# Performance work log

Measured on AMD Instinct MI355X. Metric: run time of the kernel, lower is better.

## Reference

```python
import jax, jax.numpy as jnp
import numpy as np

WIN = 7
SIZE = 56
HEADS = 16
DIM = 512
SHIFT = WIN // 2  # 3


def _rel_index():
    # Matches torch.meshgrid (ij) + flatten + pairwise diff indexing of the bias table.
    coords = np.stack(np.meshgrid(np.arange(WIN), np.arange(WIN), indexing='ij')).reshape(2, -1)  # [2,49]
    rel = (coords[:, :, None] - coords[:, None, :]).transpose(1, 2, 0)  # [49,49,2]
    rel[..., 0] += WIN - 1
    rel[..., 1] += WIN - 1
    rel[..., 0] *= 2 * WIN - 1
    return (rel[..., 0] + rel[..., 1]).reshape(-1)  # [49*49]


def _attn_mask():
    # Shifted-window mask: windows mixing different regions get -100 on cross pairs.
    img = np.zeros((SIZE, SIZE))
    sl = (slice(0, -WIN), slice(-WIN, -SHIFT), slice(-SHIFT, None))
    cnt = 0
    for h in sl:
        for w in sl:
            img[h, w] = cnt
            cnt += 1
    m = img.reshape(SIZE // WIN, WIN, SIZE // WIN, WIN).transpose(0, 2, 1, 3).reshape(-1, WIN * WIN)  # [nW,49]
    am = m[:, None, :] - m[:, :, None]  # [nW,49,49]
    return np.where(am != 0, -100.0, 0.0).astype(np.float32)


_REL_IDX = _rel_index()
_MASK = _attn_mask()  # [64,49,49]


def setup_inputs() -> dict:
    key = jax.random.key(0)
    ks = jax.random.split(key, 6)
    Bn, N, C = 2048, WIN * WIN, DIM
    return {
        'x': jax.random.normal(ks[0], (Bn, N, C), jnp.float32),
        'qkv_w': jax.random.normal(ks[1], (C, 3 * C), jnp.float32) * (C ** -0.5),
        'qkv_b': jax.random.normal(ks[2], (3 * C,), jnp.float32) * 0.02,
        'proj_w': jax.random.normal(ks[3], (C, C), jnp.float32) * (C ** -0.5),
        'proj_b': jax.random.normal(ks[4], (C,), jnp.float32) * 0.02,
        'bias_table': jax.random.normal(ks[5], ((2 * WIN - 1) ** 2, HEADS), jnp.float32) * 0.02,
    }


def reference(x, qkv_w, qkv_b, proj_w, proj_b, bias_table):
    Bn, N, C = x.shape
    D = C // HEADS
    qkv = (x @ qkv_w + qkv_b).reshape(Bn, N, 3, HEADS, D).transpose(2, 0, 3, 1, 4)  # [3,Bn,H,N,D]
    q, k, v = qkv[0] * (D ** -0.5), qkv[1], qkv[2]
    attn = jnp.einsum('bhnd,bhmd->bhnm', q, k)  # [Bn,H,N,N]
    bias = bias_table[jnp.asarray(_REL_IDX)].reshape(N, N, HEADS).transpose(2, 0, 1)  # [H,N,N]
    attn = attn + bias[None]
    mask = jnp.asarray(_MASK, x.dtype)  # [nW,N,N]
    nW = mask.shape[0]
    attn = attn.reshape(Bn // nW, nW, HEADS, N, N) + mask[None, :, None]
    attn = jax.nn.softmax(attn.reshape(Bn, HEADS, N, N), axis=-1)
    out = jnp.einsum('bhnm,bhmd->bhnd', attn, v).transpose(0, 2, 1, 3).reshape(Bn, N, C)
    return out @ proj_w + proj_b
```

## Files before the change

### kernel.cpp

```cpp
#include <hip/hip_runtime.h>
#include <hip/hip_bf16.h>
#include <stdint.h>


#define HEADS 16
#define NTOK  49
#define CH    512

typedef float  f32x4  __attribute__((ext_vector_type(4)));
typedef __bf16 bf16x8 __attribute__((ext_vector_type(8)));
typedef unsigned short u16;
typedef unsigned int   u32;

__device__ __forceinline__ u16 f2bf(float f) {
  return __builtin_bit_cast(u16, (__bf16)f);
}

__device__ __forceinline__ void gload16(const u16* g, u16* l) {
  __builtin_amdgcn_global_load_lds(
      (const __attribute__((address_space(1))) u32*)g,
      (__attribute__((address_space(3))) u32*)l, 16, 0, 0);
}

__global__ __launch_bounds__(256) void k_wprep(const float* __restrict__ qkv_w,
                                               const float* __restrict__ proj_w,
                                               const float* __restrict__ qkv_b,
                                               u16* __restrict__ Wt, u16* __restrict__ Pt,
                                               float* __restrict__ bias2) {
  const float sc = 0.17677669529663687f;
  int tid = blockIdx.x * 256 + threadIdx.x;
  const int T1 = 1536 * 512;
  if (tid < 1536) bias2[tid] = qkv_b[tid] * (tid < 512 ? sc : 1.f);
  if (tid < T1) {
    int n = tid >> 9, k = tid & 511;
    float v = qkv_w[k * 1536 + n];
    if (n < 512) v *= sc;
    Wt[tid] = f2bf(v);
  } else {
    int t2 = tid - T1;
    int n = t2 >> 9, k = t2 & 511;
    Pt[t2] = f2bf(proj_w[k * 512 + n]);
  }
}

__global__ __launch_bounds__(256) void k_xcast(const float* __restrict__ x,
                                               u16* __restrict__ xb) {
  int tid = blockIdx.x * 256 + threadIdx.x;
  const float4* xv = (const float4*)x;
  float4 a = xv[tid * 2], b = xv[tid * 2 + 1];
  u16 o[8] = {f2bf(a.x), f2bf(a.y), f2bf(a.z), f2bf(a.w),
              f2bf(b.x), f2bf(b.y), f2bf(b.z), f2bf(b.w)};
  ((int4*)xb)[tid] = *(const int4*)o;
}

__global__ __launch_bounds__(256) void k_tabs(const float* __restrict__ bias_table,
                                              float* __restrict__ biasM,
                                              float* __restrict__ maskT) {
  int tid = blockIdx.x * 256 + threadIdx.x;
  if (tid < 16 * 4096) {
    int h = tid >> 12, rc = tid & 4095, r = rc >> 6, c = rc & 63;
    float v = -1e30f;
    if (r < NTOK && c < NTOK) {
      int ih = r / 7, iw = r - ih * 7, jh = c / 7, jw = c - jh * 7;
      v = bias_table[((ih - jh + 6) * 13 + (iw - jw + 6)) * HEADS + h];
    }
    biasM[tid] = v;
  } else {
    int t2 = tid - 65536;
    int mw = t2 >> 12, rc = t2 & 4095, r = rc >> 6, c = rc & 63;
    float v = 0.f;
    if (r < NTOK && c < NTOK) {
      int mwR = (mw >> 3) * 7, mwC = (mw & 7) * 7;
      int ih = r / 7, iw = r - ih * 7, jh = c / 7, jw = c - jh * 7;
      int gih = mwR + ih, giw = mwC + iw, gjh = mwR + jh, gjw = mwC + jw;
      int ri = (gih < 49 ? 0 : (gih < 53 ? 1 : 2)) * 3 + (giw < 49 ? 0 : (giw < 53 ? 1 : 2));
      int rj = (gjh < 49 ? 0 : (gjh < 53 ? 1 : 2)) * 3 + (gjw < 49 ? 0 : (gjw < 53 ? 1 : 2));
      v = (ri != rj) ? -100.f : 0.f;
    }
    maskT[t2] = v;
  }
}

template<int OUT_F32>
__global__ __launch_bounds__(512, 2) void k_gemm(const u16* __restrict__ A,
                                                 const u16* __restrict__ Bt,
                                                 const float* __restrict__ bias,
                                                 void* __restrict__ Cp,
                                                 int M, int Nn, int K, int nbn) {
  __shared__ u16 smem[2 * 32768];
  const int t   = threadIdx.x;
  const int q8  = gridDim.x >> 3;
  const int bid = (blockIdx.x & 7) * q8 + (blockIdx.x >> 3);
  const int cb  = bid % nbn, rb = bid / nbn;
  const int row0 = rb << 8, col0 = cb << 8;
  const int lane = t & 63, w = t >> 6;
  const int wr = (w >> 2) & 1, wc = w & 3;
  const int lm = lane & 15, lk = lane >> 4;

  const f32x4 fz = {0.f, 0.f, 0.f, 0.f};
  f32x4 acc[8][4];
#pragma unroll
  for (int i = 0; i < 8; i++)
#pragma unroll
    for (int j = 0; j < 4; j++) acc[i][j] = fz;

  int gr[4], gc[4], gdb[4];
#pragma unroll
  for (int i = 0; i < 4; ++i) {
    int q = (i << 9) + t;
    gr[i]  = q >> 3;
    gc[i]  = (((q & 7) ^ (gr[i] & 7)) << 3);
    gdb[i] = (i << 12) + ((t & 448) << 3);
  }
  int offA[8], offB[4];
#pragma unroll
  for (int i = 0; i < 8; ++i) {
    int rowA = (wr << 7) + i * 16 + lm;
    offA[i] = rowA * 64 + ((lk ^ (rowA & 7)) << 3);
  }
#pragma unroll
  for (int i = 0; i < 4; ++i) {
    int rowB = (wc << 6) + i * 16 + lm;
    offB[i] = rowB * 64 + ((lk ^ (rowB & 7)) << 3);
  }

  auto stage = [&](int p, int kt) {
    const int kb = kt << 6;
    u16* dA = smem + p * 32768;
    u16* dB = dA + 16384;
#pragma unroll
    for (int i = 0; i < 4; ++i) {
      gload16(A  + (size_t)(row0 + gr[i]) * K + kb + gc[i], dA + gdb[i]);
      gload16(Bt + (size_t)(col0 + gr[i]) * K + kb + gc[i], dB + gdb[i]);
    }
  };

  const int nk = K >> 6;
  stage(0, 0);
  int p = 0;
  for (int kt = 0; kt < nk; ++kt) {
    if (kt + 1 < nk) {
      stage(p ^ 1, kt + 1);
      asm volatile("s_waitcnt vmcnt(8)" ::: "memory");
    } else {
      asm volatile("s_waitcnt vmcnt(0)" ::: "memory");
    }
    __builtin_amdgcn_s_barrier();
    asm volatile("" ::: "memory");
    const u16* sA = smem + p * 32768;
    const u16* sB = sA + 16384;
#pragma unroll
    for (int kk = 0; kk < 2; ++kk) {
      bf16x8 a[8], b[4];
#pragma unroll
      for (int mi = 0; mi < 8; ++mi)
        a[mi] = *(const bf16x8*)(sA + (offA[mi] ^ (kk << 5)));
#pragma unroll
      for (int ni = 0; ni < 4; ++ni)
        b[ni] = *(const bf16x8*)(sB + (offB[ni] ^ (kk << 5)));
#pragma unroll
      for (int mi = 0; mi < 8; ++mi)
#pragma unroll
        for (int ni = 0; ni < 4; ++ni)
          acc[mi][ni] = __builtin_amdgcn_mfma_f32_16x16x32_bf16(a[mi], b[ni],
                                                                acc[mi][ni], 0, 0, 0);
    }
    asm volatile("" ::: "memory");
    __builtin_amdgcn_s_barrier();
    asm volatile("" ::: "memory");
    p ^= 1;
  }

  if constexpr (!OUT_F32) {
    for (int half = 0; half < 2; ++half) {
      __syncthreads();
      if (wr == half) {
#pragma unroll
        for (int mi = 0; mi < 8; ++mi)
#pragma unroll
          for (int ni = 0; ni < 4; ++ni) {
            int col = (wc << 6) + ni * 16 + lm;
            float bv = bias[col0 + col];
#pragma unroll
            for (int r = 0; r < 4; ++r)
              smem[(mi * 16 + lk * 4 + r) * 264 + col] = f2bf(acc[mi][ni][r] + bv);
          }
      }
      __syncthreads();
      const int row = t >> 2, seg = t & 3;
      u16* dst = (u16*)Cp + (size_t)(row0 + half * 128 + row) * Nn + col0 + seg * 64;
      const u16* src = smem + row * 264 + seg * 64;
#pragma unroll
      for (int i = 0; i < 8; ++i)
        *(int4*)(dst + i * 8) = *(const int4*)(src + i * 8);
    }
  } else {
    float* smf = (float*)smem;
    for (int q = 0; q < 4; ++q) {
      __syncthreads();
      if (wr == (q >> 1)) {
        const int mib = (q & 1) * 4;
#pragma unroll
        for (int mo = 0; mo < 4; ++mo)
#pragma unroll
          for (int ni = 0; ni < 4; ++ni) {
            int col = (wc << 6) + ni * 16 + lm;
            float bv = bias[col0 + col];
#pragma unroll
            for (int r = 0; r < 4; ++r)
              smf[(mo * 16 + lk * 4 + r) * 264 + col] = acc[mib + mo][ni][r] + bv;
          }
      }
      __syncthreads();
      const int row = t >> 3, seg = t & 7;
      float* dst = (float*)Cp + (size_t)(row0 + q * 64 + row) * Nn + col0 + seg * 32;
      const float* src = smf + row * 264 + seg * 32;
#pragma unroll
      for (int i = 0; i < 8; ++i)
        *(float4*)(dst + i * 4) = *(const float4*)(src + i * 4);
    }
  }
}

__global__ __launch_bounds__(256) void k_attn(const u16* __restrict__ qkv,
                                              const float* __restrict__ biasM,
                                              const float* __restrict__ maskT,
                                              u16* __restrict__ aout) {
  __shared__ u16 sm[4 * 3264];
  const int wdx = blockIdx.x;
  const int mw  = wdx & 63;
  const int t   = threadIdx.x;
  const int wv  = t >> 6;
  const int l   = t & 63;
  const int lm  = l & 15, lk = l >> 4;
  const size_t tb = (size_t)wdx * NTOK;
  const u16* base = qkv + tb * 1536;
  u16* sV = sm + wv * 3264;
  u16* sP = sV + 2176;

  const int4  iz = make_int4(0, 0, 0, 0);
  const f32x4 fz = {0.f, 0.f, 0.f, 0.f};
  const float* mT = maskT + (mw << 12);

  for (int hh = 0; hh < 4; ++hh) {
    const int h = (wv << 2) + hh;

    {
      int4 vv[4] = {iz, iz, iz, iz};
      if (l < NTOK) {
        const u16* vp = base + (size_t)l * 1536 + 1024 + h * 32;
#pragma unroll
        for (int i = 0; i < 4; ++i) vv[i] = *(const int4*)(vp + i * 8);
      }
      const u16* u = (const u16*)vv;
#pragma unroll
      for (int d = 0; d < 32; ++d) sV[d * 68 + l] = u[d];
    }

    bf16x8 kf[4];
#pragma unroll
    for (int ni = 0; ni < 4; ++ni) {
      int krow = ni * 16 + lm;
      int4 ki = (krow < NTOK)
        ? *(const int4*)(base + (size_t)krow * 1536 + 512 + h * 32 + lk * 8) : iz;
      kf[ni] = __builtin_bit_cast(bf16x8, ki);
    }

    bf16x8 vb[2][2];
#pragma unroll
    for (int kt = 0; kt < 2; ++kt)
#pragma unroll
      for (int df = 0; df < 2; ++df)
        vb[kt][df] = *(const bf16x8*)(sV + (df * 16 + lm) * 68 + kt * 32 + lk * 8);

    const float* bM = biasM + (h << 12);

#pragma unroll
    for (int mi = 0; mi < 4; ++mi) {
      const int qrow = mi * 16 + lm;
      int4 qi = (qrow < NTOK)
        ? *(const int4*)(base + (size_t)qrow * 1536 + h * 32 + lk * 8) : iz;
      bf16x8 qf = __builtin_bit_cast(bf16x8, qi);

      f32x4 st[4];
#pragma unroll
      for (int ni = 0; ni < 4; ++ni) {
        const int o4 = (qrow << 6) + ni * 16 + lk * 4;
        float4 b4 = *(const float4*)(bM + o4);
        float4 m4 = *(const float4*)(mT + o4);
        f32x4 ci = {b4.x + m4.x, b4.y + m4.y, b4.z + m4.z, b4.w + m4.w};
        st[ni] = __builtin_amdgcn_mfma_f32_16x16x32_bf16(kf[ni], qf, ci, 0, 0, 0);
      }

      float mx = -3e38f;
#pragma unroll
      for (int ni = 0; ni < 4; ++ni)
#pragma unroll
        for (int r = 0; r < 4; ++r) mx = fmaxf(mx, st[ni][r]);
      mx = fmaxf(mx, __shfl_xor(mx, 16, 64));
      mx = fmaxf(mx, __shfl_xor(mx, 32, 64));
      float sum = 0.f;
#pragma unroll
      for (int ni = 0; ni < 4; ++ni)
#pragma unroll
        for (int r = 0; r < 4; ++r) {
          float p = __expf(st[ni][r] - mx);
          st[ni][r] = p;
          sum += p;
        }
      sum += __shfl_xor(sum, 16, 64);
      sum += __shfl_xor(sum, 32, 64);
      const float rinv = __builtin_amdgcn_rcpf(sum);

#pragma unroll
      for (int ni = 0; ni < 4; ++ni) {
        u16 pk[4] = {f2bf(st[ni][0] * rinv), f2bf(st[ni][1] * rinv),
                     f2bf(st[ni][2] * rinv), f2bf(st[ni][3] * rinv)};
        *(int2*)(sP + lm * 68 + ni * 16 + lk * 4) = *(const int2*)pk;
      }

      f32x4 o0 = fz, o1 = fz;
#pragma unroll
      for (int kt = 0; kt < 2; ++kt) {
        bf16x8 pa = *(const bf16x8*)(sP + lm * 68 + kt * 32 + lk * 8);
        o0 = __builtin_amdgcn_mfma_f32_16x16x32_bf16(pa, vb[kt][0], o0, 0, 0, 0);
        o1 = __builtin_amdgcn_mfma_f32_16x16x32_bf16(pa, vb[kt][1], o1, 0, 0, 0);
      }

#pragma unroll
      for (int r = 0; r < 4; ++r) {
        int tok = mi * 16 + lk * 4 + r;
        if (tok < NTOK) {
          size_t ob = (tb + tok) * CH + h * 32;
          aout[ob + lm]      = f2bf(o0[r]);
          aout[ob + 16 + lm] = f2bf(o1[r]);
        }
      }
    }
  }
}

extern "C" void kernel_launch(void* const* d_in, const int* in_sizes, int n_in,
                              void* d_out, int out_size, void* d_ws, size_t ws_size,
                              hipStream_t stream) {
  const float* x      = (const float*)d_in[0];
  const float* qkv_b  = (const float*)d_in[2];
  const float* proj_b = (const float*)d_in[4];
  const float* btab   = (const float*)d_in[5];

  char* ws   = (char*)d_ws;
  u16* Wt    = (u16*)ws;
  u16* Pt    = (u16*)(ws + 1572864);
  u16* qkv   = (u16*)(ws + 2097152);
  u16* aout  = (u16*)(ws + 2097152 + 308281344ull);
  u16* xb    = aout;
  float* biasM = (float*)(ws + 2097152 + 308281344ull + 102760448ull);
  float* maskT = biasM + 65536;
  float* bias2 = maskT + 262144;
  float* out = (float*)d_out;

  k_wprep<<<4096, 256, 0, stream>>>((const float*)d_in[1], (const float*)d_in[3],
                                    qkv_b, Wt, Pt, bias2);
  k_xcast<<<25088, 256, 0, stream>>>(x, xb);
  k_tabs<<<1280, 256, 0, stream>>>(btab, biasM, maskT);
  k_gemm<0><<<392 * 6, 512, 0, stream>>>(xb, Wt, bias2, (void*)qkv, 100352, 1536, 512, 6);
  k_attn<<<2048, 256, 0, stream>>>(qkv, biasM, maskT, aout);
  k_gemm<1><<<392 * 2, 512, 0, stream>>>(aout, Pt, proj_b, (void*)out, 100352, 512, 512, 2);
}
```

Measured before the change: 657.9 us.

## Split GEMM k-step into four MFMA phases with staggered A/B prefetch and setprio

Restructures the bf16 GEMM main loop into four phases, each loading half of the A fragments and the B fragments from LDS before running a 4x4 MFMA block. The prefetch of the next A tile is issued at loop start and the next B tile mid-iteration. MFMA blocks are wrapped in s_setprio and sched_barrier, which aims to overlap LDS reads and global-to-LDS copies with matrix math across waves. The cost is more barriers per iteration (about eight instead of two), a finer vmcnt wait, and dependence on correct barrier ordering so B is not overwritten while still being read.

```diff
diff --git a/kernel.cpp b/kernel.cpp
--- a/kernel.cpp
+++ b/kernel.cpp
@@ -124,50 +124,113 @@
     offB[i] = rowB * 64 + ((lk ^ (rowB & 7)) << 3);
   }
 
-  auto stage = [&](int p, int kt) {
+  auto stageA = [&](int p, int kt) {
     const int kb = kt << 6;
     u16* dA = smem + p * 32768;
-    u16* dB = dA + 16384;
-#pragma unroll
-    for (int i = 0; i < 4; ++i) {
-      gload16(A  + (size_t)(row0 + gr[i]) * K + kb + gc[i], dA + gdb[i]);
+#pragma unroll
+    for (int i = 0; i < 4; ++i)
+      gload16(A + (size_t)(row0 + gr[i]) * K + kb + gc[i], dA + gdb[i]);
+  };
+  auto stageB = [&](int p, int kt) {
+    const int kb = kt << 6;
+    u16* dB = smem + p * 32768 + 16384;
+#pragma unroll
+    for (int i = 0; i < 4; ++i)
       gload16(Bt + (size_t)(col0 + gr[i]) * K + kb + gc[i], dB + gdb[i]);
-    }
   };
 
   const int nk = K >> 6;
-  stage(0, 0);
+  stageA(0, 0);
+  stageB(0, 0);
   int p = 0;
   for (int kt = 0; kt < nk; ++kt) {
+    const u16* sA = smem + p * 32768;
+    const u16* sB = sA + 16384;
+    bf16x8 aL[4], aH[4], bK[4];
+
     if (kt + 1 < nk) {
-      stage(p ^ 1, kt + 1);
-      asm volatile("s_waitcnt vmcnt(8)" ::: "memory");
+      stageA(p ^ 1, kt + 1);
+      asm volatile("s_waitcnt vmcnt(4)" ::: "memory");
     } else {
       asm volatile("s_waitcnt vmcnt(0)" ::: "memory");
     }
     __builtin_amdgcn_s_barrier();
     asm volatile("" ::: "memory");
-    const u16* sA = smem + p * 32768;
-    const u16* sB = sA + 16384;
-#pragma unroll
-    for (int kk = 0; kk < 2; ++kk) {
-      bf16x8 a[8], b[4];
-#pragma unroll
-      for (int mi = 0; mi < 8; ++mi)
-        a[mi] = *(const bf16x8*)(sA + (offA[mi] ^ (kk << 5)));
-#pragma unroll
-      for (int ni = 0; ni < 4; ++ni)
-        b[ni] = *(const bf16x8*)(sB + (offB[ni] ^ (kk << 5)));
-#pragma unroll
-      for (int mi = 0; mi < 8; ++mi)
-#pragma unroll
-        for (int ni = 0; ni < 4; ++ni)
-          acc[mi][ni] = __builtin_amdgcn_mfma_f32_16x16x32_bf16(a[mi], b[ni],
-                                                                acc[mi][ni], 0, 0, 0);
-    }
-    asm volatile("" ::: "memory");
-    __builtin_amdgcn_s_barrier();
-    asm volatile("" ::: "memory");
+#pragma unroll
+    for (int i = 0; i < 4; ++i) aL[i] = *(const bf16x8*)(sA + offA[i]);
+#pragma unroll
+    for (int i = 0; i < 4; ++i) bK[i] = *(const bf16x8*)(sB + offB[i]);
+    asm volatile("s_waitcnt lgkmcnt(0)" ::: "memory");
+    __builtin_amdgcn_sched_barrier(0);
+    __builtin_amdgcn_s_setprio(1);
+#pragma unroll
+    for (int mi = 0; mi < 4; ++mi)
+#pragma unroll
+      for (int ni = 0; ni < 4; ++ni)
+        acc[mi][ni] = __builtin_amdgcn_mfma_f32_16x16x32_bf16(aL[mi], bK[ni],
+                                                              acc[mi][ni], 0, 0, 0);
+    __builtin_amdgcn_s_setprio(0);
+    asm volatile("" ::: "memory");
+    __builtin_amdgcn_s_barrier();
+    asm volatile("" ::: "memory");
+
+#pragma unroll
+    for (int i = 0; i < 4; ++i) aH[i] = *(const bf16x8*)(sA + offA[4 + i]);
+    if (kt + 1 < nk) stageB(p ^ 1, kt + 1);
+    asm volatile("" ::: "memory");
+    __builtin_amdgcn_s_barrier();
+    asm volatile("s_waitcnt lgkmcnt(0)" ::: "memory");
+    __builtin_amdgcn_sched_barrier(0);
+    __builtin_amdgcn_s_setprio(1);
+#pragma unroll
+    for (int mi = 0; mi < 4; ++mi)
+#pragma unroll
+      for (int ni = 0; ni < 4; ++ni)
+        acc[4 + mi][ni] = __builtin_amdgcn_mfma_f32_16x16x32_bf16(aH[mi], bK[ni],
+                                                                  acc[4 + mi][ni], 0, 0, 0);
+    __builtin_amdgcn_s_setprio(0);
+    asm volatile("" ::: "memory");
+    __builtin_amdgcn_s_barrier();
+    asm volatile("" ::: "memory");
+
+#pragma unroll
+    for (int i = 0; i < 4; ++i) aL[i] = *(const bf16x8*)(sA + (offA[i] ^ 32));
+#pragma unroll
+    for (int i = 0; i < 4; ++i) bK[i] = *(const bf16x8*)(sB + (offB[i] ^ 32));
+    asm volatile("" ::: "memory");
+    __builtin_amdgcn_s_barrier();
+    asm volatile("s_waitcnt lgkmcnt(0)" ::: "memory");
+    __builtin_amdgcn_sched_barrier(0);
+    __builtin_amdgcn_s_setprio(1);
+#pragma unroll
+    for (int mi = 0; mi < 4; ++mi)
+#pragma unroll
+      for (int ni = 0; ni < 4; ++ni)
+        acc[mi][ni] = __builtin_amdgcn_mfma_f32_16x16x32_bf16(aL[mi], bK[ni],
+                                                              acc[mi][ni], 0, 0, 0);
+    __builtin_amdgcn_s_setprio(0);
+    asm volatile("" ::: "memory");
+    __builtin_amdgcn_s_barrier();
+    asm volatile("" ::: "memory");
+
+#pragma unroll
+    for (int i = 0; i < 4; ++i) aH[i] = *(const bf16x8*)(sA + (offA[4 + i] ^ 32));
+    asm volatile("" ::: "memory");
+    __builtin_amdgcn_s_barrier();
+    asm volatile("s_waitcnt lgkmcnt(0)" ::: "memory");
+    __builtin_amdgcn_sched_barrier(0);
+    __builtin_amdgcn_s_setprio(1);
+#pragma unroll
+    for (int mi = 0; mi < 4; ++mi)
+#pragma unroll
+      for (int ni = 0; ni < 4; ++ni)
+        acc[4 + mi][ni] = __builtin_amdgcn_mfma_f32_16x16x32_bf16(aH[mi], bK[ni],
+                                                                  acc[4 + mi][ni], 0, 0, 0);
+    __builtin_amdgcn_s_setprio(0);
+    asm volatile("" ::: "memory");
+    __builtin_amdgcn_s_barrier();
+    asm volatile("" ::: "memory");
+
     p ^= 1;
   }
 
```

Measured after the change: 666.1 us. About the same (+1.3%).
